# Kernel tuning notes

Hardware: AMD Instinct MI355X
Metric: run time of the kernel (lower is better)

## Reference

```python
import jax, jax.numpy as jnp
import numpy as np

B, H, W, CIN, COUT, KH, KW = 16, 64, 64, 256, 256, 3, 3


def setup_inputs() -> dict:
    key = jax.random.key(0)
    k1, k2, k3 = jax.random.split(key, 3)
    x = jax.random.normal(k1, (B, H, W, CIN), dtype=jnp.float32)
    style = jax.random.normal(k2, (B, CIN), dtype=jnp.float32)
    # glorot-ish scale for the base kernel
    kernel = jax.random.normal(k3, (KH, KW, CIN, COUT), dtype=jnp.float32) * 0.05
    return {"x": x, "style": style, "kernel": kernel}


def reference(x, style, kernel):
    b = x.shape[0]
    cout = kernel.shape[-1]
    # Modulate: per-sample weights [B, kh, kw, Cin, Cout]
    w = kernel[None] * (style[:, None, None, :, None] + 1.0)
    # Demodulate: L2 normalize over (kh, kw, Cin) per (sample, out-channel)
    w = w / jnp.sqrt(jnp.sum(jnp.square(w), axis=(1, 2, 3), keepdims=True) + 1e-8)
    # Batch-as-groups grouped conv: x -> [1, B*Cin, H, W]
    xg = jnp.transpose(x, (0, 3, 1, 2)).reshape(1, -1, x.shape[1], x.shape[2])
    # w -> [kh, kw, Cin, B*Cout]
    wg = jnp.transpose(w, (1, 2, 3, 0, 4)).reshape(w.shape[1], w.shape[2], w.shape[3], -1)
    y = jax.lax.conv_general_dilated(
        xg, wg,
        window_strides=(1, 1),
        padding='SAME',
        dimension_numbers=('NCHW', 'HWIO', 'NCHW'),
        feature_group_count=b,
    )
    # [1, B*Cout, H, W] -> [B, H, W, Cout]
    y = y.reshape(b, cout, y.shape[2], y.shape[3])
    return jnp.transpose(y, (0, 2, 3, 1))
```

## Files before the change

### kernel.cpp

```cpp
#include <hip/hip_runtime.h>


#define HH 64
#define WW 64
#define CI 256
#define CO 256
#define KTOT 2304
#define CIPITCH 40
#define XCOLS 66
#define BPITCH 100

typedef float    f32x4 __attribute__((ext_vector_type(4)));
typedef _Float16 f16x8 __attribute__((ext_vector_type(8)));
typedef __fp16   fp16x2 __attribute__((ext_vector_type(2)));

__device__ __forceinline__ unsigned pk2(float a, float b) {
    fp16x2 h = __builtin_amdgcn_cvt_pkrtz(a, b);
    return __builtin_bit_cast(unsigned, h);
}

__global__ __launch_bounds__(256) void modscale_part(
    const float* __restrict__ kern,
    const float* __restrict__ style,
    float* __restrict__ scale2)
{
    const int b = blockIdx.x / 9;
    const int t = blockIdx.x - b * 9;
    const int tid = threadIdx.x;
    __shared__ float st[CI];
    st[tid] = style[b * CI + tid] + 1.0f;
    __syncthreads();
    float acc = 0.f;
    const float* kp = kern + (size_t)t * CI * CO + tid;
    #pragma unroll 8
    for (int ci = 0; ci < CI; ++ci) {
        float m = kp[ci * CO] * st[ci];
        acc += m * m;
    }
    atomicAdd(&scale2[b * CO + tid], acc);
}

__global__ __launch_bounds__(256) void prep_wt(const float* __restrict__ kern,
                                               ushort* __restrict__ Wt) {
    __shared__ ushort tile[64][65];
    const int kt = blockIdx.x >> 2;
    const int ct = blockIdx.x & 3;
    const int k0 = kt * 64, c0 = ct * 64;
    const int tid = threadIdx.x;
    const int r = tid >> 2, q = tid & 3;

    const float* src = kern + (size_t)(k0 + r) * CO + c0 + q * 16;
    #pragma unroll
    for (int j = 0; j < 16; ++j) {
        _Float16 h = (_Float16)src[j];
        tile[q * 16 + j][r] = __builtin_bit_cast(unsigned short, h);
    }
    __syncthreads();
    ushort* dst = Wt + (size_t)(c0 + r) * KTOT + k0 + q * 16;
    #pragma unroll
    for (int j = 0; j < 16; ++j) dst[j] = tile[r][q * 16 + j];
}

__global__ __launch_bounds__(256) void gemm_conv(
    const float* __restrict__ x,
    const ushort* __restrict__ Wt,
    const float* __restrict__ style,
    const float* __restrict__ scale2,
    float* __restrict__ y)
{
    __shared__ __align__(16) ushort xs[4 * XCOLS * CIPITCH];
    __shared__ __align__(16) ushort bs[128 * BPITCH];
    __shared__ float s_style[CI];

    const int tid  = threadIdx.x;
    const int lane = tid & 63;
    const int wave = tid >> 6;

    const int mtile = blockIdx.x >> 1;
    const int n0    = (blockIdx.x & 1) * 128;
    const int p0    = mtile * 128;
    const int b     = p0 >> 12;
    const int h0    = (p0 >> 6) & 63;

    s_style[tid] = style[b * CI + tid] + 1.0f;

    const int wm = (wave & 1) * 64;
    const int wn = (wave >> 1) * 64;
    const int fr = lane & 15;
    const int fq = lane >> 4;
    const int xlane = fr * CIPITCH + fq * 8;

    f32x4 acc[4][4] = {};

    for (int c = 0; c < 8; ++c) {
        __syncthreads();

        #pragma unroll
        for (int p = 0; p < 9; ++p) {
            const int task = p * 256 + tid;
            if (task < 2112) {
                const int rowcol = task >> 3;
                const int chunk  = task & 7;
                const int row = rowcol / XCOLS;
                const int col = rowcol - row * XCOLS;
                const int rg = h0 - 1 + row;
                const int cg = col - 1;
                f32x4 v = {0.f, 0.f, 0.f, 0.f};
                if ((unsigned)rg < 64u && (unsigned)cg < 64u)
                    v = *(const f32x4*)(x + ((size_t)((b * HH + rg) * WW + cg)) * CI
                                          + c * 32 + chunk * 4);
                const f32x4 st = *(const f32x4*)(s_style + c * 32 + chunk * 4);
                const f32x4 m = v * st;
                uint2 u;
                u.x = pk2(m.x, m.y);
                u.y = pk2(m.z, m.w);
                *(uint2*)(xs + rowcol * CIPITCH + chunk * 4) = u;
            }
        }

        #pragma unroll
        for (int tr = 0; tr < 3; ++tr) {
            if (tr) __syncthreads();

            #pragma unroll
            for (int p = 0; p < 6; ++p) {
                const int task = p * 256 + tid;
                const int co = task / 12;
                const int r  = task - co * 12;
                const int tl = r >> 2;
                const int ch = r & 3;
                const uint4 v = *(const uint4*)(Wt + (size_t)(n0 + co) * KTOT
                                                + (tr * 3 + tl) * 256 + c * 32 + ch * 8);
                *(uint4*)(bs + co * BPITCH + tl * 32 + ch * 8) = v;
            }
            __syncthreads();

            #pragma unroll
            for (int tl = 0; tl < 3; ++tl) {
                const int t  = tr * 3 + tl;
                const int dh = t / 3;
                const int dw = t - dh * 3;

                f16x8 af[4], bf[4];
                #pragma unroll
                for (int i = 0; i < 4; ++i) {
                    const int mb   = wm + i * 16;
                    const int mrow = (mb >> 6) + dh;
                    const int mcol = (mb & 63) + dw;
                    af[i] = *(const f16x8*)(xs + (mrow * XCOLS + mcol) * CIPITCH + xlane);
                }
                #pragma unroll
                for (int j = 0; j < 4; ++j)
                    bf[j] = *(const f16x8*)(bs + (wn + j * 16 + fr) * BPITCH
                                            + tl * 32 + fq * 8);
                #pragma unroll
                for (int i = 0; i < 4; ++i)
                    #pragma unroll
                    for (int j = 0; j < 4; ++j)
                        acc[i][j] = __builtin_amdgcn_mfma_f32_16x16x32_f16(
                            af[i], bf[j], acc[i][j], 0, 0, 0);
            }
        }
    }

    float sc[4];
    #pragma unroll
    for (int j = 0; j < 4; ++j)
        sc[j] = __frsqrt_rn(scale2[b * CO + n0 + wn + j * 16 + fr] + 1e-8f);
    #pragma unroll
    for (int i = 0; i < 4; ++i) {
        const int m_base = p0 + wm + i * 16 + fq * 4;
        #pragma unroll
        for (int j = 0; j < 4; ++j) {
            float* yp = y + (size_t)m_base * CO + n0 + wn + j * 16 + fr;
            #pragma unroll
            for (int r = 0; r < 4; ++r)
                yp[(size_t)r * CO] = acc[i][j][r] * sc[j];
        }
    }
}

extern "C" void kernel_launch(void* const* d_in, const int* in_sizes, int n_in,
                              void* d_out, int out_size, void* d_ws, size_t ws_size,
                              hipStream_t stream) {
    const float* x     = (const float*)d_in[0];
    const float* style = (const float*)d_in[1];
    const float* kern  = (const float*)d_in[2];
    float* out = (float*)d_out;

    float*  scale2 = (float*)d_ws;
    ushort* Wt     = (ushort*)((char*)d_ws + 16384);

    hipMemsetAsync(scale2, 0, 16 * CO * sizeof(float), stream);
    modscale_part<<<16 * 9, 256, 0, stream>>>(kern, style, scale2);
    prep_wt<<<144, 256, 0, stream>>>(kern, Wt);
    gemm_conv<<<512 * 2, 256, 0, stream>>>(x, Wt, style, scale2, out);
}
```

Measured before the change: 244.3 us.

## Fuse prep kernels, prefetch x into registers, remap blocks, lighten barriers

Result: slower. 354.4 us (+45.1%).

```diff
diff --git a/kernel.cpp b/kernel.cpp
--- a/kernel.cpp
+++ b/kernel.cpp
@@ -8,7 +8,7 @@
 #define KTOT 2304
 #define CIPITCH 40
 #define XCOLS 66
-#define BPITCH 100
+#define BPITCH 104
 
 typedef float    f32x4 __attribute__((ext_vector_type(4)));
 typedef _Float16 f16x8 __attribute__((ext_vector_type(8)));
@@ -19,49 +19,66 @@
     return __builtin_bit_cast(unsigned, h);
 }
 
-__global__ __launch_bounds__(256) void modscale_part(
+#define BAR() do { \
+    asm volatile("s_waitcnt lgkmcnt(0)" ::: "memory"); \
+    __builtin_amdgcn_s_barrier(); \
+} while (0)
+
+__global__ __launch_bounds__(256) void prep(
     const float* __restrict__ kern,
     const float* __restrict__ style,
+    ushort* __restrict__ Wt,
     float* __restrict__ scale2)
 {
-    const int b = blockIdx.x / 9;
-    const int t = blockIdx.x - b * 9;
-    const int tid = threadIdx.x;
-    __shared__ float st[CI];
-    st[tid] = style[b * CI + tid] + 1.0f;
-    __syncthreads();
-    float acc = 0.f;
-    const float* kp = kern + (size_t)t * CI * CO + tid;
-    #pragma unroll 8
-    for (int ci = 0; ci < CI; ++ci) {
-        float m = kp[ci * CO] * st[ci];
-        acc += m * m;
-    }
-    atomicAdd(&scale2[b * CO + tid], acc);
-}
-
-__global__ __launch_bounds__(256) void prep_wt(const float* __restrict__ kern,
-                                               ushort* __restrict__ Wt) {
     __shared__ ushort tile[64][65];
+    __shared__ float  sqt[64][65];
+    __shared__ float  st2l[16][64];
+
     const int kt = blockIdx.x >> 2;
     const int ct = blockIdx.x & 3;
     const int k0 = kt * 64, c0 = ct * 64;
+    const int ci0 = k0 & 255;
     const int tid = threadIdx.x;
     const int r = tid >> 2, q = tid & 3;
 
+    #pragma unroll
+    for (int p = 0; p < 4; ++p) {
+        const int i = p * 256 + tid;
+        const int bb = i >> 6, rr = i & 63;
+        const float s = style[bb * CI + ci0 + rr] + 1.0f;
+        st2l[bb][rr] = s * s;
+    }
+
     const float* src = kern + (size_t)(k0 + r) * CO + c0 + q * 16;
     #pragma unroll
     for (int j = 0; j < 16; ++j) {
-        _Float16 h = (_Float16)src[j];
+        const float v = src[j];
+        _Float16 h = (_Float16)v;
         tile[q * 16 + j][r] = __builtin_bit_cast(unsigned short, h);
+        sqt[r][q * 16 + j] = v * v;
     }
     __syncthreads();
+
     ushort* dst = Wt + (size_t)(c0 + r) * KTOT + k0 + q * 16;
     #pragma unroll
     for (int j = 0; j < 16; ++j) dst[j] = tile[r][q * 16 + j];
-}
-
-__global__ __launch_bounds__(256) void gemm_conv(
+
+    const int co = tid & 63;
+    const int bq = tid >> 6;
+    float acc[4] = {0.f, 0.f, 0.f, 0.f};
+    #pragma unroll 4
+    for (int rr = 0; rr < 64; ++rr) {
+        const float s = sqt[rr][co];
+        #pragma unroll
+        for (int bb = 0; bb < 4; ++bb)
+            acc[bb] += s * st2l[bq * 4 + bb][rr];
+    }
+    #pragma unroll
+    for (int bb = 0; bb < 4; ++bb)
+        atomicAdd(&scale2[(bq * 4 + bb) * CO + c0 + co], acc[bb]);
+}
+
+__global__ __launch_bounds__(256, 3) void gemm_conv(
     const float* __restrict__ x,
     const ushort* __restrict__ Wt,
     const float* __restrict__ style,
@@ -76,8 +93,9 @@
     const int lane = tid & 63;
     const int wave = tid >> 6;
 
-    const int mtile = blockIdx.x >> 1;
-    const int n0    = (blockIdx.x & 1) * 128;
+    const int nbid  = ((blockIdx.x & 7) << 7) | (blockIdx.x >> 3);
+    const int mtile = nbid >> 1;
+    const int n0    = (nbid & 1) * 128;
     const int p0    = mtile * 128;
     const int b     = p0 >> 12;
     const int h0    = (p0 >> 6) & 63;
@@ -90,10 +108,32 @@
     const int fq = lane >> 4;
     const int xlane = fr * CIPITCH + fq * 8;
 
+    int xoff[9];
+    #pragma unroll
+    for (int p = 0; p < 9; ++p) {
+        const int task = p * 256 + tid;
+        const int rowcol = task >> 3;
+        const int chunk  = task & 7;
+        const int row = rowcol / XCOLS;
+        const int col = rowcol - row * XCOLS;
+        const int rg = h0 - 1 + row;
+        const int cg = col - 1;
+        xoff[p] = ((unsigned)rg < 64u && (unsigned)cg < 64u && task < 2112)
+                  ? (((b * HH + rg) * WW + cg) * CI + chunk * 4) : -1;
+    }
+
     f32x4 acc[4][4] = {};
+    f32x4 xv[9];
+
+    #pragma unroll
+    for (int p = 0; p < 9; ++p) {
+        f32x4 v = {0.f, 0.f, 0.f, 0.f};
+        if (xoff[p] >= 0) v = *(const f32x4*)(x + xoff[p]);
+        xv[p] = v;
+    }
 
     for (int c = 0; c < 8; ++c) {
-        __syncthreads();
+        BAR();
 
         #pragma unroll
         for (int p = 0; p < 9; ++p) {
@@ -101,16 +141,8 @@
             if (task < 2112) {
                 const int rowcol = task >> 3;
                 const int chunk  = task & 7;
-                const int row = rowcol / XCOLS;
-                const int col = rowcol - row * XCOLS;
-                const int rg = h0 - 1 + row;
-                const int cg = col - 1;
-                f32x4 v = {0.f, 0.f, 0.f, 0.f};
-                if ((unsigned)rg < 64u && (unsigned)cg < 64u)
-                    v = *(const f32x4*)(x + ((size_t)((b * HH + rg) * WW + cg)) * CI
-                                          + c * 32 + chunk * 4);
                 const f32x4 st = *(const f32x4*)(s_style + c * 32 + chunk * 4);
-                const f32x4 m = v * st;
+                const f32x4 m = xv[p] * st;
                 uint2 u;
                 u.x = pk2(m.x, m.y);
                 u.y = pk2(m.z, m.w);
@@ -118,9 +150,18 @@
             }
         }
 
+        if (c < 7) {
+            #pragma unroll
+            for (int p = 0; p < 9; ++p) {
+                f32x4 v = {0.f, 0.f, 0.f, 0.f};
+                if (xoff[p] >= 0) v = *(const f32x4*)(x + xoff[p] + (c + 1) * 32);
+                xv[p] = v;
+            }
+        }
+
         #pragma unroll
         for (int tr = 0; tr < 3; ++tr) {
-            if (tr) __syncthreads();
+            if (tr) BAR();
 
             #pragma unroll
             for (int p = 0; p < 6; ++p) {
@@ -133,7 +174,7 @@
                                                 + (tr * 3 + tl) * 256 + c * 32 + ch * 8);
                 *(uint4*)(bs + co * BPITCH + tl * 32 + ch * 8) = v;
             }
-            __syncthreads();
+            BAR();
 
             #pragma unroll
             for (int tl = 0; tl < 3; ++tl) {
@@ -192,7 +233,6 @@
     ushort* Wt     = (ushort*)((char*)d_ws + 16384);
 
     hipMemsetAsync(scale2, 0, 16 * CO * sizeof(float), stream);
-    modscale_part<<<16 * 9, 256, 0, stream>>>(kern, style, scale2);
-    prep_wt<<<144, 256, 0, stream>>>(kern, Wt);
+    prep<<<144, 256, 0, stream>>>(kern, style, Wt, scale2);
     gemm_conv<<<512 * 2, 256, 0, stream>>>(x, Wt, style, scale2, out);
 }
```
